# Kernel optimization log

Hardware: AMD Instinct MI355X
Metric: run time of the kernel (lower is better)

Reference implementation:

```python
import jax, jax.numpy as jnp
import numpy as np

D_MODEL = 1024
D_FF = 4096
FFN_H = int(2 * D_FF / 3)  # 2730, per SwiGLUMLP
B, S = 4, 4096
LN_EPS = 1e-5
ATTN_EPS = 1e-6


def layer_norm(x, g, b):
    mu = jnp.mean(x, axis=-1, keepdims=True)
    var = jnp.mean(jnp.square(x - mu), axis=-1, keepdims=True)
    return (x - mu) * jax.lax.rsqrt(var + LN_EPS) * g + b


def setup_inputs() -> dict:
    key = jax.random.key(0)
    ks = jax.random.split(key, 16)
    s = 0.02
    return {
        "x": jax.random.normal(ks[0], (B, S, D_MODEL), dtype=jnp.float32),
        "Wqkv": jax.random.normal(ks[1], (D_MODEL, 3 * D_MODEL), dtype=jnp.float32) * s,
        "bqkv": jnp.zeros((3 * D_MODEL,), jnp.float32),
        "Wg": jax.random.normal(ks[2], (D_MODEL, FFN_H), dtype=jnp.float32) * s,
        "bg": jnp.zeros((FFN_H,), jnp.float32),
        "Wu": jax.random.normal(ks[3], (D_MODEL, FFN_H), dtype=jnp.float32) * s,
        "bu": jnp.zeros((FFN_H,), jnp.float32),
        "Wd": jax.random.normal(ks[4], (FFN_H, D_MODEL), dtype=jnp.float32) * s,
        "bd": jnp.zeros((D_MODEL,), jnp.float32),
        "g1": jnp.ones((D_MODEL,), jnp.float32),
        "b1": jnp.zeros((D_MODEL,), jnp.float32),
        "g2": jnp.ones((D_MODEL,), jnp.float32),
        "b2": jnp.zeros((D_MODEL,), jnp.float32),
    }


def reference(x, Wqkv, bqkv, Wg, bg, Wu, bu, Wd, bd, g1, b1, g2, b2):
    # QKV projection, split into q, k, v (each [B,S,D])
    qkv = jnp.einsum("bsd,de->bse", x, Wqkv) + bqkv
    q, k, v = jnp.split(qkv, 3, axis=-1)

    # Linear attention with elu(x)+1 feature map (non-causal)
    qp = jax.nn.elu(q) + 1.0
    kp = jax.nn.elu(k) + 1.0
    kv = jnp.einsum("bsd,bse->bde", kp, v)        # [B,D,D] context
    num = jnp.einsum("bsd,bde->bse", qp, kv)       # [B,S,D]
    k_sum = jnp.sum(kp, axis=1)                    # [B,D]
    den = jnp.einsum("bsd,bd->bs", qp, k_sum)[..., None]
    attn = num / (den + ATTN_EPS)

    x = layer_norm(x + attn, g1, b1)

    # SwiGLU MLP
    gate = jnp.einsum("bsd,dh->bsh", x, Wg) + bg
    up = jnp.einsum("bsd,dh->bsh", x, Wu) + bu
    ffn = jnp.einsum("bsh,hd->bsd", jax.nn.silu(gate) * up, Wd) + bd

    return layer_norm(x + ffn, g2, b2)
```

## Files before the change

### kernel.cpp

```cpp
#include <hip/hip_runtime.h>

#define SEQ 4096
#define TOK 16384
#define DM 1024
#define NQKV 3072
#define FFH 2730
#define FFHP 2816

typedef __bf16 bf16x8 __attribute__((ext_vector_type(8)));
typedef float f32x4 __attribute__((ext_vector_type(4)));

__device__ __forceinline__ unsigned short f2bf(float f) {
  union { float f; unsigned u; } v; v.f = f;
  unsigned r = v.u + 0x7fffu + ((v.u >> 16) & 1u);
  return (unsigned short)(r >> 16);
}
__device__ __forceinline__ float bf2f(unsigned short h) {
  union { unsigned u; float f; } v; v.u = ((unsigned)h) << 16;
  return v.f;
}

__device__ __forceinline__ void xcd_swizzle(int& bx, int& by) {
  const int gx = gridDim.x, gy = gridDim.y;
  const int chunk = gy >> 3;
  const int csh = __ffs(chunk) - 1;
  const int lin = by * gx + bx;
  const int xcd = lin & 7, j = lin >> 3;
  by = xcd * chunk + (j & (chunk - 1));
  bx = j >> csh;
}

enum { M_QKV = 0, M_BF16 = 1, M_NUM = 2, M_BIAS_F32 = 5 };

template<int MODE>
__global__ __launch_bounds__(256)
void gemm_kernel(const unsigned short* __restrict__ A,
                 const unsigned short* __restrict__ BT,
                 int K, int lda, int ldb, int ldc,
                 long zsA, long zsB, long zsC,
                 void* __restrict__ out0, void* __restrict__ out1, void* __restrict__ out2,
                 const float* __restrict__ bias, int nbias)
{
  __shared__ unsigned short As[2][128 * 64];
  __shared__ unsigned short Bs[2][128 * 64];
  const int tid  = threadIdx.x;
  const int wave = tid >> 6, lane = tid & 63;
  const int quad = lane >> 4, l16 = lane & 15;
  const int bz = blockIdx.z;
  int bx = blockIdx.x, by = blockIdx.y;
  xcd_swizzle(bx, by);

  const unsigned short* Ab = A + (size_t)zsA * bz + (size_t)by * 128 * lda;
  const unsigned short* Bb = BT + (size_t)zsB * bz + (size_t)bx * 128 * ldb;

  f32x4 acc[4][4] = {};

  const int srow   = lane >> 3;
  const int scol_g = (((lane & 7) ^ srow) * 8);
  const int axor   = l16 & 7;

  auto stage = [&](int buf, int k0) {
#pragma unroll
    for (int j = 0; j < 4; ++j) {
      int c = wave * 4 + j;
      const unsigned short* sa = Ab + (size_t)(c * 8 + srow) * lda + k0 + scol_g;
      __builtin_amdgcn_global_load_lds((__attribute__((address_space(1))) void*)sa,
          (__attribute__((address_space(3))) void*)(As[buf] + c * 512), 16, 0, 0);
      const unsigned short* sb = Bb + (size_t)(c * 8 + srow) * ldb + k0 + scol_g;
      __builtin_amdgcn_global_load_lds((__attribute__((address_space(1))) void*)sb,
          (__attribute__((address_space(3))) void*)(Bs[buf] + c * 512), 16, 0, 0);
    }
  };

  const int NIT = K >> 6;
  stage(0, 0);
  int cur = 0;
  for (int it = 0; it < NIT; ++it) {
    __builtin_amdgcn_s_waitcnt(0);
    __syncthreads();
    if (it + 1 < NIT) stage(cur ^ 1, (it + 1) << 6);
#pragma unroll
    for (int kk = 0; kk < 64; kk += 32) {
      bf16x8 af[4], bfr[4];
#pragma unroll
      for (int mt = 0; mt < 4; ++mt)
        af[mt] = *(const bf16x8*)(As[cur] + ((wave >> 1) * 64 + mt * 16 + l16) * 64
                                     + ((((kk >> 3) + quad) ^ axor) * 8));
#pragma unroll
      for (int nt = 0; nt < 4; ++nt)
        bfr[nt] = *(const bf16x8*)(Bs[cur] + ((wave & 1) * 64 + nt * 16 + l16) * 64
                                      + ((((kk >> 3) + quad) ^ axor) * 8));
#pragma unroll
      for (int mt = 0; mt < 4; ++mt)
#pragma unroll
        for (int nt = 0; nt < 4; ++nt)
          acc[mt][nt] = __builtin_amdgcn_mfma_f32_16x16x32_bf16(af[mt], bfr[nt], acc[mt][nt], 0, 0, 0);
    }
    cur ^= 1;
  }

#pragma unroll
  for (int mt = 0; mt < 4; ++mt) {
#pragma unroll
    for (int nt = 0; nt < 4; ++nt) {
      const int r0 = by * 128 + (wave >> 1) * 64 + mt * 16 + quad * 4;
      const int c  = bx * 128 + (wave & 1) * 64 + nt * 16 + l16;
      float vals[4];
#pragma unroll
      for (int i = 0; i < 4; ++i) vals[i] = acc[mt][nt][i];

      if (MODE == M_QKV) {
        const int b = r0 >> 12, s0 = r0 & 4095;
#pragma unroll
        for (int i = 0; i < 4; ++i) vals[i] += bias[c];
        if (c < 1024) {
#pragma unroll
          for (int i = 0; i < 4; ++i) {
            float e = vals[i] > 0.f ? vals[i] + 1.f : __expf(vals[i]);
            ((unsigned short*)out0)[(size_t)(r0 + i) * DM + c] = f2bf(e);
          }
        } else if (c < 2048) {
          ushort4 o;
          float e0 = vals[0] > 0.f ? vals[0] + 1.f : __expf(vals[0]);
          float e1 = vals[1] > 0.f ? vals[1] + 1.f : __expf(vals[1]);
          float e2 = vals[2] > 0.f ? vals[2] + 1.f : __expf(vals[2]);
          float e3 = vals[3] > 0.f ? vals[3] + 1.f : __expf(vals[3]);
          o.x = f2bf(e0); o.y = f2bf(e1); o.z = f2bf(e2); o.w = f2bf(e3);
          *(ushort4*)((unsigned short*)out1 + (size_t)b * DM * SEQ + (size_t)(c - 1024) * SEQ + s0) = o;
        } else {
          ushort4 o;
          o.x = f2bf(vals[0]); o.y = f2bf(vals[1]); o.z = f2bf(vals[2]); o.w = f2bf(vals[3]);
          *(ushort4*)((unsigned short*)out2 + (size_t)b * DM * SEQ + (size_t)(c - 2048) * SEQ + s0) = o;
        }
      } else {
#pragma unroll
        for (int i = 0; i < 4; ++i) {
          const int r = r0 + i;
          float val = vals[i];
          if (MODE == M_BF16 || MODE == M_NUM) {
            ((unsigned short*)out0)[(size_t)zsC * bz + (size_t)r * ldc + c] = f2bf(val);
          } else {
            if (c < nbias) val += bias[c];
            ((float*)out0)[(size_t)r * ldc + c] = val;
          }
        }
      }
    }
  }
}

__global__ __launch_bounds__(256)
void gateup_kernel(const unsigned short* __restrict__ A,
                   const unsigned short* __restrict__ BgT,
                   const unsigned short* __restrict__ BuT,
                   const float* __restrict__ bg, const float* __restrict__ bu,
                   unsigned short* __restrict__ h)
{
  __shared__ unsigned short As[2][128 * 64];
  __shared__ unsigned short Bgs[2][64 * 64];
  __shared__ unsigned short Bus[2][64 * 64];
  const int tid  = threadIdx.x;
  const int wave = tid >> 6, lane = tid & 63;
  const int quad = lane >> 4, l16 = lane & 15;
  const int wm = wave >> 1, wn = wave & 1;
  int bx = blockIdx.x, by = blockIdx.y;
  xcd_swizzle(bx, by);

  const unsigned short* Ab  = A + (size_t)by * 128 * DM;
  const unsigned short* Bgb = BgT + (size_t)bx * 64 * DM;
  const unsigned short* Bub = BuT + (size_t)bx * 64 * DM;

  f32x4 accg[4][2] = {};
  f32x4 accu[4][2] = {};

  const int srow   = lane >> 3;
  const int scol_g = (((lane & 7) ^ srow) * 8);
  const int axor   = l16 & 7;

  auto stage = [&](int buf, int k0) {
#pragma unroll
    for (int j = 0; j < 4; ++j) {
      int c = wave * 4 + j;
      const unsigned short* sa = Ab + (size_t)(c * 8 + srow) * DM + k0 + scol_g;
      __builtin_amdgcn_global_load_lds((__attribute__((address_space(1))) void*)sa,
          (__attribute__((address_space(3))) void*)(As[buf] + c * 512), 16, 0, 0);
    }
#pragma unroll
    for (int j = 0; j < 2; ++j) {
      int c = wave * 2 + j;
      const unsigned short* sg = Bgb + (size_t)(c * 8 + srow) * DM + k0 + scol_g;
      __builtin_amdgcn_global_load_lds((__attribute__((address_space(1))) void*)sg,
          (__attribute__((address_space(3))) void*)(Bgs[buf] + c * 512), 16, 0, 0);
      const unsigned short* su = Bub + (size_t)(c * 8 + srow) * DM + k0 + scol_g;
      __builtin_amdgcn_global_load_lds((__attribute__((address_space(1))) void*)su,
          (__attribute__((address_space(3))) void*)(Bus[buf] + c * 512), 16, 0, 0);
    }
  };

  const int NIT = DM >> 6;
  stage(0, 0);
  int cur = 0;
  for (int it = 0; it < NIT; ++it) {
    __builtin_amdgcn_s_waitcnt(0);
    __syncthreads();
    if (it + 1 < NIT) stage(cur ^ 1, (it + 1) << 6);
#pragma unroll
    for (int kk = 0; kk < 64; kk += 32) {
      const int kb = (((kk >> 3) + quad) ^ axor) * 8;
      bf16x8 af[4], bgf[2], buf_[2];
#pragma unroll
      for (int mt = 0; mt < 4; ++mt)
        af[mt] = *(const bf16x8*)(As[cur] + (wm * 64 + mt * 16 + l16) * 64 + kb);
#pragma unroll
      for (int nt = 0; nt < 2; ++nt) {
        bgf[nt]  = *(const bf16x8*)(Bgs[cur] + (wn * 32 + nt * 16 + l16) * 64 + kb);
        buf_[nt] = *(const bf16x8*)(Bus[cur] + (wn * 32 + nt * 16 + l16) * 64 + kb);
      }
#pragma unroll
      for (int mt = 0; mt < 4; ++mt)
#pragma unroll
        for (int nt = 0; nt < 2; ++nt) {
          accg[mt][nt] = __builtin_amdgcn_mfma_f32_16x16x32_bf16(af[mt], bgf[nt],  accg[mt][nt], 0, 0, 0);
          accu[mt][nt] = __builtin_amdgcn_mfma_f32_16x16x32_bf16(af[mt], buf_[nt], accu[mt][nt], 0, 0, 0);
        }
    }
    cur ^= 1;
  }

#pragma unroll
  for (int mt = 0; mt < 4; ++mt) {
#pragma unroll
    for (int nt = 0; nt < 2; ++nt) {
      const int r0 = by * 128 + wm * 64 + mt * 16 + quad * 4;
      const int c  = bx * 64 + wn * 32 + nt * 16 + l16;
      const float bgv = (c < FFH) ? bg[c] : 0.f;
      const float buv = (c < FFH) ? bu[c] : 0.f;
#pragma unroll
      for (int i = 0; i < 4; ++i) {
        float g = accg[mt][nt][i] + bgv;
        float u = accu[mt][nt][i] + buv;
        float hv = g / (1.f + __expf(-g)) * u;
        h[(size_t)(r0 + i) * FFHP + c] = f2bf(hv);
      }
    }
  }
}

__global__ __launch_bounds__(256)
void cvt_kernel(const float* __restrict__ in, unsigned short* __restrict__ out, int n)
{
  int i = (blockIdx.x * 256 + threadIdx.x) * 4;
  if (i < n) {
    float4 v = *(const float4*)(in + i);
    ushort4 o;
    o.x = f2bf(v.x); o.y = f2bf(v.y); o.z = f2bf(v.z); o.w = f2bf(v.w);
    *(ushort4*)(out + i) = o;
  }
}

__global__ __launch_bounds__(256)
void wtrans_kernel(const float* __restrict__ in, unsigned short* __restrict__ out,
                   int R, int C, int Cpad, int Rpad)
{
  __shared__ float tile[32][33];
  int r0 = blockIdx.x * 32;
  int c0 = blockIdx.y * 32;
  int tid = threadIdx.x;
#pragma unroll
  for (int j = 0; j < 4; ++j) {
    int r = j * 8 + (tid >> 5), c = tid & 31;
    float v = 0.f;
    if (r0 + r < R && c0 + c < C) v = in[(size_t)(r0 + r) * C + c0 + c];
    tile[r][c] = v;
  }
  __syncthreads();
#pragma unroll
  for (int j = 0; j < 4; ++j) {
    int c = j * 8 + (tid >> 5), r = tid & 31;
    out[(size_t)(c0 + c) * Rpad + (r0 + r)] = f2bf(tile[r][c]);
  }
}

__device__ __forceinline__ float block_sum(float v, float* sm)
{
#pragma unroll
  for (int o = 32; o > 0; o >>= 1) v += __shfl_down(v, o, 64);
  int w = threadIdx.x >> 6;
  if ((threadIdx.x & 63) == 0) sm[w] = v;
  __syncthreads();
  float r = sm[0] + sm[1] + sm[2] + sm[3];
  __syncthreads();
  return r;
}

__global__ __launch_bounds__(256)
void ksum_kernel(const unsigned short* __restrict__ kpT, float* __restrict__ ksum)
{
  __shared__ float sm[4];
  int row = blockIdx.x;
  const ushort4* src = (const ushort4*)(kpT + (size_t)row * SEQ);
  float s = 0.f;
#pragma unroll
  for (int j = 0; j < 4; ++j) {
    ushort4 v = src[threadIdx.x + j * 256];
    s += bf2f(v.x) + bf2f(v.y) + bf2f(v.z) + bf2f(v.w);
  }
  float tot = block_sum(s, sm);
  if (threadIdx.x == 0) ksum[row] = tot;
}

__global__ __launch_bounds__(256)
void ln1_kernel(const unsigned short* __restrict__ xb16, const unsigned short* __restrict__ num16,
                const unsigned short* __restrict__ qp, const float* __restrict__ ksum,
                const float* __restrict__ g1, const float* __restrict__ b1,
                unsigned short* __restrict__ yb)
{
  __shared__ float sm[4];
  int t = blockIdx.x, tid = threadIdx.x, b = t >> 12;
  ushort4 xv = ((const ushort4*)(xb16 + (size_t)t * DM))[tid];
  ushort4 nv = ((const ushort4*)(num16 + (size_t)t * DM))[tid];
  ushort4 qv = ((const ushort4*)(qp + (size_t)t * DM))[tid];
  float4 kv = ((const float4*)(ksum + (size_t)b * DM))[tid];
  float q0 = bf2f(qv.x), q1 = bf2f(qv.y), q2 = bf2f(qv.z), q3 = bf2f(qv.w);
  float den = block_sum(q0 * kv.x + q1 * kv.y + q2 * kv.z + q3 * kv.w, sm);
  float inv = 1.f / (den + 1e-6f);
  float r0 = bf2f(xv.x) + bf2f(nv.x) * inv, r1 = bf2f(xv.y) + bf2f(nv.y) * inv;
  float r2 = bf2f(xv.z) + bf2f(nv.z) * inv, r3 = bf2f(xv.w) + bf2f(nv.w) * inv;
  float s1 = block_sum(r0 + r1 + r2 + r3, sm);
  float s2 = block_sum(r0 * r0 + r1 * r1 + r2 * r2 + r3 * r3, sm);
  float mu = s1 * (1.f / 1024.f);
  float var = s2 * (1.f / 1024.f) - mu * mu;
  float rs = rsqrtf(var + 1e-5f);
  float4 gv = ((const float4*)g1)[tid];
  float4 bv = ((const float4*)b1)[tid];
  ushort4 o;
  o.x = f2bf((r0 - mu) * rs * gv.x + bv.x);
  o.y = f2bf((r1 - mu) * rs * gv.y + bv.y);
  o.z = f2bf((r2 - mu) * rs * gv.z + bv.z);
  o.w = f2bf((r3 - mu) * rs * gv.w + bv.w);
  ((ushort4*)(yb + (size_t)t * DM))[tid] = o;
}

__global__ __launch_bounds__(256)
void ln2_kernel(const unsigned short* __restrict__ yb, const float* __restrict__ ffn,
                const float* __restrict__ g2, const float* __restrict__ b2,
                float* __restrict__ out)
{
  __shared__ float sm[4];
  int t = blockIdx.x, tid = threadIdx.x;
  ushort4 yv = ((const ushort4*)(yb + (size_t)t * DM))[tid];
  float4 fv = ((const float4*)(ffn + (size_t)t * DM))[tid];
  float r0 = bf2f(yv.x) + fv.x, r1 = bf2f(yv.y) + fv.y;
  float r2 = bf2f(yv.z) + fv.z, r3 = bf2f(yv.w) + fv.w;
  float s1 = block_sum(r0 + r1 + r2 + r3, sm);
  float s2 = block_sum(r0 * r0 + r1 * r1 + r2 * r2 + r3 * r3, sm);
  float mu = s1 * (1.f / 1024.f);
  float var = s2 * (1.f / 1024.f) - mu * mu;
  float rs = rsqrtf(var + 1e-5f);
  float4 gv = ((const float4*)g2)[tid];
  float4 bv = ((const float4*)b2)[tid];
  float4 o;
  o.x = (r0 - mu) * rs * gv.x + bv.x;
  o.y = (r1 - mu) * rs * gv.y + bv.y;
  o.z = (r2 - mu) * rs * gv.z + bv.z;
  o.w = (r3 - mu) * rs * gv.w + bv.w;
  ((float4*)(out + (size_t)t * DM))[tid] = o;
}

extern "C" void kernel_launch(void* const* d_in, const int* in_sizes, int n_in,
                              void* d_out, int out_size, void* d_ws, size_t ws_size,
                              hipStream_t stream)
{
  const float* x    = (const float*)d_in[0];
  const float* Wqkv = (const float*)d_in[1];
  const float* bqkv = (const float*)d_in[2];
  const float* Wg   = (const float*)d_in[3];
  const float* bg   = (const float*)d_in[4];
  const float* Wu   = (const float*)d_in[5];
  const float* bu   = (const float*)d_in[6];
  const float* Wd   = (const float*)d_in[7];
  const float* bd   = (const float*)d_in[8];
  const float* g1   = (const float*)d_in[9];
  const float* b1   = (const float*)d_in[10];
  const float* g2   = (const float*)d_in[11];
  const float* b2   = (const float*)d_in[12];
  float* out = (float*)d_out;

  char* ws = (char*)d_ws;
  size_t off = 0;
  auto alloc = [&](size_t bytes) {
    char* p = ws + off;
    off += (bytes + 255) & ~(size_t)255;
    return p;
  };
  unsigned short* WqkvT = (unsigned short*)alloc((size_t)NQKV * DM * 2);
  unsigned short* WgT   = (unsigned short*)alloc((size_t)FFHP * DM * 2);
  unsigned short* WuT   = (unsigned short*)alloc((size_t)FFHP * DM * 2);
  unsigned short* WdT   = (unsigned short*)alloc((size_t)DM * FFHP * 2);
  float*          ksum  = (float*)alloc((size_t)4 * DM * 4);
  unsigned short* xbyb  = (unsigned short*)alloc((size_t)TOK * DM * 2);
  unsigned short* kvT   = (unsigned short*)alloc((size_t)4 * DM * DM * 2);
  char* R3 = alloc((size_t)3 * TOK * DM * 2);
  unsigned short* qp  = (unsigned short*)(R3);
  unsigned short* kpT = (unsigned short*)(R3 + (size_t)TOK * DM * 2);
  unsigned short* vT  = (unsigned short*)(R3 + (size_t)2 * TOK * DM * 2);
  unsigned short* hbuf = (unsigned short*)(R3);
  unsigned short* xb = xbyb;
  unsigned short* yb = xbyb;
  unsigned short* num = (unsigned short*)d_out;
  float* ffn = (float*)d_out;

  dim3 blk(256);

  cvt_kernel<<<dim3(TOK * DM / 1024), blk, 0, stream>>>(x, xb, TOK * DM);
  wtrans_kernel<<<dim3(32, 96), blk, 0, stream>>>(Wqkv, WqkvT, 1024, 3072, 3072, 1024);
  wtrans_kernel<<<dim3(32, 88), blk, 0, stream>>>(Wg, WgT, 1024, FFH, FFHP, 1024);
  wtrans_kernel<<<dim3(32, 88), blk, 0, stream>>>(Wu, WuT, 1024, FFH, FFHP, 1024);
  wtrans_kernel<<<dim3(88, 32), blk, 0, stream>>>(Wd, WdT, FFH, 1024, 1024, FFHP);
  gemm_kernel<M_QKV><<<dim3(NQKV / 128, TOK / 128), blk, 0, stream>>>(
      xb, WqkvT, 1024, 1024, 1024, 0, 0, 0, 0, qp, kpT, vT, bqkv, NQKV);
  ksum_kernel<<<dim3(4096), blk, 0, stream>>>(kpT, ksum);
  gemm_kernel<M_BF16><<<dim3(8, 8, 4), blk, 0, stream>>>(
      vT, kpT, 4096, 4096, 4096, 1024,
      (long)DM * SEQ, (long)DM * SEQ, (long)DM * DM,
      kvT, nullptr, nullptr, nullptr, 0);
  gemm_kernel<M_NUM><<<dim3(8, 32, 4), blk, 0, stream>>>(
      qp, kvT, 1024, 1024, 1024, 1024,
      (long)SEQ * DM, (long)DM * DM, (long)SEQ * DM,
      num, nullptr, nullptr, nullptr, 0);
  ln1_kernel<<<dim3(TOK), blk, 0, stream>>>(xb, num, qp, ksum, g1, b1, yb);
  gateup_kernel<<<dim3(FFHP / 64, TOK / 128), blk, 0, stream>>>(
      yb, WgT, WuT, bg, bu, hbuf);
  gemm_kernel<M_BIAS_F32><<<dim3(DM / 128, TOK / 128), blk, 0, stream>>>(
      hbuf, WdT, FFHP, FFHP, FFHP, DM, 0, 0, 0, ffn, nullptr, nullptr, bd, DM);
  ln2_kernel<<<dim3(TOK), blk, 0, stream>>>(yb, ffn, g2, b2, out);

  (void)in_sizes; (void)n_in; (void)out_size; (void)ws_size;
}
```

Baseline: 832.3 us.

## Load B operand fragments directly from global into registers, bypassing LDS

Result: slower. 1.277 ms (+53.4%).

```diff
diff --git a/kernel.cpp b/kernel.cpp
--- a/kernel.cpp
+++ b/kernel.cpp
@@ -42,7 +42,6 @@
                  const float* __restrict__ bias, int nbias)
 {
   __shared__ unsigned short As[2][128 * 64];
-  __shared__ unsigned short Bs[2][128 * 64];
   const int tid  = threadIdx.x;
   const int wave = tid >> 6, lane = tid & 63;
   const int quad = lane >> 4, l16 = lane & 15;
@@ -59,43 +58,56 @@
   const int scol_g = (((lane & 7) ^ srow) * 8);
   const int axor   = l16 & 7;
 
-  auto stage = [&](int buf, int k0) {
+  auto stageA = [&](int buf, int k0) {
 #pragma unroll
     for (int j = 0; j < 4; ++j) {
       int c = wave * 4 + j;
       const unsigned short* sa = Ab + (size_t)(c * 8 + srow) * lda + k0 + scol_g;
       __builtin_amdgcn_global_load_lds((__attribute__((address_space(1))) void*)sa,
           (__attribute__((address_space(3))) void*)(As[buf] + c * 512), 16, 0, 0);
-      const unsigned short* sb = Bb + (size_t)(c * 8 + srow) * ldb + k0 + scol_g;
-      __builtin_amdgcn_global_load_lds((__attribute__((address_space(1))) void*)sb,
-          (__attribute__((address_space(3))) void*)(Bs[buf] + c * 512), 16, 0, 0);
     }
   };
 
+  const unsigned short* Brow[4];
+#pragma unroll
+  for (int nt = 0; nt < 4; ++nt)
+    Brow[nt] = Bb + (size_t)((wave & 1) * 64 + nt * 16 + l16) * ldb + quad * 8;
+
   const int NIT = K >> 6;
-  stage(0, 0);
+  bf16x8 bcur[8], bnxt[8];
+  stageA(0, 0);
+#pragma unroll
+  for (int h = 0; h < 2; ++h)
+#pragma unroll
+    for (int nt = 0; nt < 4; ++nt)
+      bcur[h * 4 + nt] = *(const bf16x8*)(Brow[nt] + h * 32);
+
   int cur = 0;
   for (int it = 0; it < NIT; ++it) {
     __builtin_amdgcn_s_waitcnt(0);
     __syncthreads();
-    if (it + 1 < NIT) stage(cur ^ 1, (it + 1) << 6);
+    if (it + 1 < NIT) stageA(cur ^ 1, (it + 1) << 6);
+    const int knl = ((it + 1 < NIT) ? (it + 1) : it) << 6;
+#pragma unroll
+    for (int h = 0; h < 2; ++h)
+#pragma unroll
+      for (int nt = 0; nt < 4; ++nt)
+        bnxt[h * 4 + nt] = *(const bf16x8*)(Brow[nt] + knl + h * 32);
 #pragma unroll
     for (int kk = 0; kk < 64; kk += 32) {
-      bf16x8 af[4], bfr[4];
+      bf16x8 af[4];
 #pragma unroll
       for (int mt = 0; mt < 4; ++mt)
         af[mt] = *(const bf16x8*)(As[cur] + ((wave >> 1) * 64 + mt * 16 + l16) * 64
                                      + ((((kk >> 3) + quad) ^ axor) * 8));
 #pragma unroll
-      for (int nt = 0; nt < 4; ++nt)
-        bfr[nt] = *(const bf16x8*)(Bs[cur] + ((wave & 1) * 64 + nt * 16 + l16) * 64
-                                      + ((((kk >> 3) + quad) ^ axor) * 8));
-#pragma unroll
       for (int mt = 0; mt < 4; ++mt)
 #pragma unroll
         for (int nt = 0; nt < 4; ++nt)
-          acc[mt][nt] = __builtin_amdgcn_mfma_f32_16x16x32_bf16(af[mt], bfr[nt], acc[mt][nt], 0, 0, 0);
-    }
+          acc[mt][nt] = __builtin_amdgcn_mfma_f32_16x16x32_bf16(af[mt], bcur[(kk >> 5) * 4 + nt], acc[mt][nt], 0, 0, 0);
+    }
+#pragma unroll
+    for (int i = 0; i < 8; ++i) bcur[i] = bnxt[i];
     cur ^= 1;
   }
 
@@ -157,8 +169,6 @@
                    unsigned short* __restrict__ h)
 {
   __shared__ unsigned short As[2][128 * 64];
-  __shared__ unsigned short Bgs[2][64 * 64];
-  __shared__ unsigned short Bus[2][64 * 64];
   const int tid  = threadIdx.x;
   const int wave = tid >> 6, lane = tid & 63;
   const int quad = lane >> 4, l16 = lane & 15;
@@ -167,8 +177,6 @@
   xcd_swizzle(bx, by);
 
   const unsigned short* Ab  = A + (size_t)by * 128 * DM;
-  const unsigned short* Bgb = BgT + (size_t)bx * 64 * DM;
-  const unsigned short* Bub = BuT + (size_t)bx * 64 * DM;
 
   f32x4 accg[4][2] = {};
   f32x4 accu[4][2] = {};
@@ -177,7 +185,7 @@
   const int scol_g = (((lane & 7) ^ srow) * 8);
   const int axor   = l16 & 7;
 
-  auto stage = [&](int buf, int k0) {
+  auto stageA = [&](int buf, int k0) {
 #pragma unroll
     for (int j = 0; j < 4; ++j) {
       int c = wave * 4 + j;
@@ -185,45 +193,52 @@
       __builtin_amdgcn_global_load_lds((__attribute__((address_space(1))) void*)sa,
           (__attribute__((address_space(3))) void*)(As[buf] + c * 512), 16, 0, 0);
     }
-#pragma unroll
-    for (int j = 0; j < 2; ++j) {
-      int c = wave * 2 + j;
-      const unsigned short* sg = Bgb + (size_t)(c * 8 + srow) * DM + k0 + scol_g;
-      __builtin_amdgcn_global_load_lds((__attribute__((address_space(1))) void*)sg,
-          (__attribute__((address_space(3))) void*)(Bgs[buf] + c * 512), 16, 0, 0);
-      const unsigned short* su = Bub + (size_t)(c * 8 + srow) * DM + k0 + scol_g;
-      __builtin_amdgcn_global_load_lds((__attribute__((address_space(1))) void*)su,
-          (__attribute__((address_space(3))) void*)(Bus[buf] + c * 512), 16, 0, 0);
-    }
   };
 
+  const unsigned short* Brow[4];
+#pragma unroll
+  for (int nt = 0; nt < 2; ++nt) {
+    Brow[nt]     = BgT + (size_t)(bx * 64 + wn * 32 + nt * 16 + l16) * DM + quad * 8;
+    Brow[2 + nt] = BuT + (size_t)(bx * 64 + wn * 32 + nt * 16 + l16) * DM + quad * 8;
+  }
+
   const int NIT = DM >> 6;
-  stage(0, 0);
+  bf16x8 bcur[8], bnxt[8];
+  stageA(0, 0);
+#pragma unroll
+  for (int h2 = 0; h2 < 2; ++h2)
+#pragma unroll
+    for (int q = 0; q < 4; ++q)
+      bcur[h2 * 4 + q] = *(const bf16x8*)(Brow[q] + h2 * 32);
+
   int cur = 0;
   for (int it = 0; it < NIT; ++it) {
     __builtin_amdgcn_s_waitcnt(0);
     __syncthreads();
-    if (it + 1 < NIT) stage(cur ^ 1, (it + 1) << 6);
+    if (it + 1 < NIT) stageA(cur ^ 1, (it + 1) << 6);
+    const int knl = ((it + 1 < NIT) ? (it + 1) : it) << 6;
+#pragma unroll
+    for (int h2 = 0; h2 < 2; ++h2)
+#pragma unroll
+      for (int q = 0; q < 4; ++q)
+        bnxt[h2 * 4 + q] = *(const bf16x8*)(Brow[q] + knl + h2 * 32);
 #pragma unroll
     for (int kk = 0; kk < 64; kk += 32) {
       const int kb = (((kk >> 3) + quad) ^ axor) * 8;
-      bf16x8 af[4], bgf[2], buf_[2];
+      bf16x8 af[4];
 #pragma unroll
       for (int mt = 0; mt < 4; ++mt)
         af[mt] = *(const bf16x8*)(As[cur] + (wm * 64 + mt * 16 + l16) * 64 + kb);
 #pragma unroll
-      for (int nt = 0; nt < 2; ++nt) {
-        bgf[nt]  = *(const bf16x8*)(Bgs[cur] + (wn * 32 + nt * 16 + l16) * 64 + kb);
-        buf_[nt] = *(const bf16x8*)(Bus[cur] + (wn * 32 + nt * 16 + l16) * 64 + kb);
-      }
-#pragma unroll
       for (int mt = 0; mt < 4; ++mt)
 #pragma unroll
         for (int nt = 0; nt < 2; ++nt) {
-          accg[mt][nt] = __builtin_amdgcn_mfma_f32_16x16x32_bf16(af[mt], bgf[nt],  accg[mt][nt], 0, 0, 0);
-          accu[mt][nt] = __builtin_amdgcn_mfma_f32_16x16x32_bf16(af[mt], buf_[nt], accu[mt][nt], 0, 0, 0);
+          accg[mt][nt] = __builtin_amdgcn_mfma_f32_16x16x32_bf16(af[mt], bcur[(kk >> 5) * 4 + nt],     accg[mt][nt], 0, 0, 0);
+          accu[mt][nt] = __builtin_amdgcn_mfma_f32_16x16x32_bf16(af[mt], bcur[(kk >> 5) * 4 + 2 + nt], accu[mt][nt], 0, 0, 0);
         }
     }
+#pragma unroll
+    for (int i = 0; i < 8; ++i) bcur[i] = bnxt[i];
     cur ^= 1;
   }
 
```
